# Kernel optimization log

Measured on AMD Instinct MI355X. Metric: run time of the kernel, lower is better.

## Reference

```python
import jax, jax.numpy as jnp
import numpy as np

TOPK = 10  # keep N // TOPK largest scores per query row
EPS = 1e-10


def setup_inputs() -> dict:
    key = jax.random.key(0)
    ks = jax.random.split(key, 8)
    B, C, H, W = 4, 64, 64, 64
    KD, OD = 32, 64  # key_dim, out_dim (out_dim must equal C for residual/view)
    x = jax.random.normal(ks[0], (B, C, H, W), jnp.float32)
    s = 0.05
    Wq = jax.random.normal(ks[1], (KD, C), jnp.float32) * s
    bq = jax.random.normal(ks[2], (KD,), jnp.float32) * s
    Wk = jax.random.normal(ks[3], (KD, C), jnp.float32) * s
    bk = jax.random.normal(ks[4], (KD,), jnp.float32) * s
    Wv = jax.random.normal(ks[5], (OD, C), jnp.float32) * s
    bv = jax.random.normal(ks[6], (OD,), jnp.float32) * s
    gamma = jnp.full((1,), 0.5, jnp.float32)  # torch init is 0; nonzero so output != x
    return {"x": x, "Wq": Wq, "bq": bq, "Wk": Wk, "bk": bk, "Wv": Wv, "bv": bv, "gamma": gamma}


def reference(x, Wq, bq, Wk, bk, Wv, bv, gamma):
    B, C, H, W = x.shape
    N = H * W
    xf = x.reshape(B, C, N)
    # 1x1 convs == per-pixel linear projections
    q = jnp.einsum('kc,bcn->bnk', Wq, xf) + bq                 # [B, N, KD]
    k = jnp.einsum('kc,bcn->bkn', Wk, xf) + bk[:, None]        # [B, KD, N]
    v = jnp.einsum('vc,bcn->bvn', Wv, xf) + bv[:, None]        # [B, OD, N]
    energy = jnp.einsum('bnk,bkm->bnm', q, k)                  # [B, N, N]
    kk = N // TOPK
    _, idx = jax.lax.top_k(energy, kk)                         # [B, N, kk]
    # scatter 1.0 at top-k positions along last dim
    bi = jnp.arange(B)[:, None, None]
    ri = jnp.arange(N)[None, :, None]
    mask = jnp.zeros_like(energy).at[bi, ri, idx].set(1.0)
    # mask_softmax: max over FULL row (matches torch code), exp, mask, renormalize
    m = jnp.max(energy, axis=-1, keepdims=True)
    e = jnp.exp(energy - m) * mask
    attn = e / (jnp.sum(e, axis=-1, keepdims=True) + EPS)      # [B, N, N]
    # bmm(value, attention^T): out[b,v,i] = sum_j v[b,v,j] * attn[b,i,j]
    out = jnp.einsum('bvj,bij->bvi', v, attn)                  # [B, OD, N]
    return (gamma[0] * out + xf).reshape(B, C, H, W)
```

## Files before the change

### kernel.cpp

```cpp
#include <hip/hip_runtime.h>

#define BATCH 4
#define CCH   64
#define NPIX  4096
#define KD    32
#define OD    64
#define KK    409
#define EPSF  1e-10f

__global__ __launch_bounds__(256, 4) void qkv_kernel(
    const float* __restrict__ x,
    const float* __restrict__ Wq, const float* __restrict__ bq,
    const float* __restrict__ Wk, const float* __restrict__ bk,
    const float* __restrict__ Wv, const float* __restrict__ bv,
    float* __restrict__ Q, float* __restrict__ Km, float* __restrict__ Vm)
{
    __shared__ float xt[64][65];
    __shared__ float wat[64][36];
    __shared__ float wbt[64][36];
    __shared__ float ba_s[32], bb_s[32];

    int tid = threadIdx.x;
    int bx  = blockIdx.x;
    bool vmode = bx >= 256;
    int tile = vmode ? bx - 256 : bx;
    int b    = tile >> 6;
    int n0   = (tile & 63) << 6;

    for (int i = tid; i < 64 * 64; i += 256) {
        int c = i >> 6, p = i & 63;
        xt[c][p] = x[((size_t)b * CCH + c) * NPIX + n0 + p];
    }
    if (!vmode) {
        for (int i = tid; i < 2048; i += 256) {
            int o = i >> 6, c = i & 63;
            wat[c][o] = Wq[i];
            wbt[c][o] = Wk[i];
        }
        if (tid < 32) { ba_s[tid] = bq[tid]; bb_s[tid] = bk[tid]; }
    } else {
        for (int i = tid; i < 4096; i += 256) {
            int o = i >> 6, c = i & 63;
            if (o < 32) wat[c][o] = Wv[i]; else wbt[c][o - 32] = Wv[i];
        }
        if (tid < 32) { ba_s[tid] = bv[tid]; bb_s[tid] = bv[tid + 32]; }
    }
    __syncthreads();

    int px  = tid & 63;
    int grp = tid >> 6;
    int n   = n0 + px;
    const float (*wt)[36] = (grp < 2) ? wat : wbt;
    const float* bs = (grp < 2) ? ba_s : bb_s;
    int o0 = (grp & 1) << 4;

    float a[16];
    #pragma unroll
    for (int t = 0; t < 16; ++t) a[t] = bs[o0 + t];

    #pragma unroll 2
    for (int c = 0; c < 64; ++c) {
        float xv = xt[c][px];
        const float4* wr = (const float4*)&wt[c][o0];
        float4 w0 = wr[0], w1 = wr[1], w2 = wr[2], w3 = wr[3];
        a[0]  = fmaf(w0.x, xv, a[0]);  a[1]  = fmaf(w0.y, xv, a[1]);
        a[2]  = fmaf(w0.z, xv, a[2]);  a[3]  = fmaf(w0.w, xv, a[3]);
        a[4]  = fmaf(w1.x, xv, a[4]);  a[5]  = fmaf(w1.y, xv, a[5]);
        a[6]  = fmaf(w1.z, xv, a[6]);  a[7]  = fmaf(w1.w, xv, a[7]);
        a[8]  = fmaf(w2.x, xv, a[8]);  a[9]  = fmaf(w2.y, xv, a[9]);
        a[10] = fmaf(w2.z, xv, a[10]); a[11] = fmaf(w2.w, xv, a[11]);
        a[12] = fmaf(w3.x, xv, a[12]); a[13] = fmaf(w3.y, xv, a[13]);
        a[14] = fmaf(w3.z, xv, a[14]); a[15] = fmaf(w3.w, xv, a[15]);
    }

    if (!vmode) {
        if (grp < 2) {
            #pragma unroll
            for (int t = 0; t < 16; ++t)
                Q[((size_t)b * NPIX + n) * KD + o0 + t] = a[t];
        } else {
            #pragma unroll
            for (int t = 0; t < 16; ++t)
                Km[((size_t)b * KD + o0 + t) * NPIX + n] = a[t];
        }
    } else {
        int ob = ((grp < 2) ? 0 : 32) + o0;
        #pragma unroll
        for (int t = 0; t < 16; ++t)
            Vm[((size_t)b * NPIX + n) * OD + ob + t] = a[t];
    }
}

__global__ __launch_bounds__(512, 4) void attn_kernel(
    const float* __restrict__ x,  const float* __restrict__ Q,
    const float* __restrict__ Km, const float* __restrict__ Vm,
    const float* __restrict__ gamma, float* __restrict__ out)
{
    __shared__ __align__(16) unsigned short ek[8][NPIX];
    __shared__ __align__(16) float qld[KD][8];
    __shared__ __align__(16) unsigned h8[8][256];
    __shared__ unsigned redk0[8][8];
    volatile __shared__ unsigned sh_b8[8], sh_r8[8];

    int tid  = threadIdx.x;
    int lane = tid & 63, wv = tid >> 6;
    int bx   = blockIdx.x;
    int b    = bx >> 9;
    int i0   = (bx & 511) << 3;

    float gscale = gamma[0];

    if (tid < 256) {
        int kd = tid & 31, rr = tid >> 5;
        qld[kd][rr] = Q[((size_t)b * NPIX + i0 + rr) * KD + kd];
    }
    __syncthreads();

    #define EKEY(EV, KV) { KV = (int)fmaf((EV), 4096.0f, 32768.0f); \
                           KV = KV < 0 ? 0 : (KV > 65535 ? 65535 : KV); }

    const float4* Kb4 = (const float4*)(Km + (size_t)b * KD * NPIX);
    unsigned lm0 = 0u, lm1 = 0u, lm2 = 0u, lm3 = 0u,
             lm4 = 0u, lm5 = 0u, lm6 = 0u, lm7 = 0u;
    #pragma unroll 1
    for (int g = 0; g < 2; ++g) {
        int c4 = tid + (g << 9);
        float4 a0 = {0,0,0,0}, a1 = {0,0,0,0}, a2 = {0,0,0,0}, a3 = {0,0,0,0};
        float4 a4 = {0,0,0,0}, a5 = {0,0,0,0}, a6 = {0,0,0,0}, a7 = {0,0,0,0};
        #pragma unroll 4
        for (int kd = 0; kd < KD; ++kd) {
            float4 kv = Kb4[(kd << 10) + c4];
            float4 qA = *(const float4*)&qld[kd][0];
            float4 qB = *(const float4*)&qld[kd][4];
            #define FMA4(A, S) { A.x = fmaf((S), kv.x, A.x); A.y = fmaf((S), kv.y, A.y); \
                                 A.z = fmaf((S), kv.z, A.z); A.w = fmaf((S), kv.w, A.w); }
            FMA4(a0, qA.x) FMA4(a1, qA.y) FMA4(a2, qA.z) FMA4(a3, qA.w)
            FMA4(a4, qB.x) FMA4(a5, qB.y) FMA4(a6, qB.z) FMA4(a7, qB.w)
            #undef FMA4
        }
        #define DOROW(A, R, LM) { int k0,k1,k2,k3; \
            EKEY(A.x,k0); EKEY(A.y,k1); EKEY(A.z,k2); EKEY(A.w,k3); \
            LM = max(LM, (unsigned)max(max(k0,k1),max(k2,k3))); \
            ((ushort4*)ek[R])[c4] = make_ushort4((unsigned short)k0,(unsigned short)k1, \
                                                 (unsigned short)k2,(unsigned short)k3); }
        DOROW(a0,0,lm0) DOROW(a1,1,lm1) DOROW(a2,2,lm2) DOROW(a3,3,lm3)
        DOROW(a4,4,lm4) DOROW(a5,5,lm5) DOROW(a6,6,lm6) DOROW(a7,7,lm7)
        #undef DOROW
    }
    #define RMAX(V, R) { unsigned v_ = (V); \
        _Pragma("unroll") \
        for (int off = 32; off; off >>= 1) \
            v_ = max(v_, (unsigned)__shfl_down((int)v_, off, 64)); \
        if (lane == 0) redk0[wv][R] = v_; }
    RMAX(lm0,0) RMAX(lm1,1) RMAX(lm2,2) RMAX(lm3,3)
    RMAX(lm4,4) RMAX(lm5,5) RMAX(lm6,6) RMAX(lm7,7)
    #undef RMAX
    __syncthreads();

    const int r = wv;
    const int i = i0 + r;
    unsigned mk = 0u;
    #pragma unroll
    for (int w = 0; w < 8; ++w) mk = max(mk, redk0[w][r]);
    const ushort4* ek4 = (const ushort4*)ek[r];
    unsigned* hw = h8[r];

    #define WSCAN(RNEED, OUTB, OUTR) { \
        uint4 hh = *((const uint4*)&hw[lane << 2]); \
        unsigned s3 = hh.w, s2 = hh.w + hh.z, s1 = s2 + hh.y, s0 = s1 + hh.x; \
        unsigned X = s0; \
        _Pragma("unroll") \
        for (int off = 1; off < 64; off <<= 1) { \
            unsigned v = (unsigned)__shfl_down((int)X, off, 64); \
            if (lane + off < 64) X += v; } \
        unsigned Xn = (unsigned)__shfl_down((int)X, 1, 64); \
        if (lane == 63) Xn = 0u; \
        unsigned S0 = X, S1 = Xn + s1, S2 = Xn + s2, S3 = Xn + s3, S4 = Xn; \
        if (S0 >= (RNEED) && S1 < (RNEED)) { sh_b8[r] = (lane << 2) | 0; sh_r8[r] = (RNEED) - S1; } \
        if (S1 >= (RNEED) && S2 < (RNEED)) { sh_b8[r] = (lane << 2) | 1; sh_r8[r] = (RNEED) - S2; } \
        if (S2 >= (RNEED) && S3 < (RNEED)) { sh_b8[r] = (lane << 2) | 2; sh_r8[r] = (RNEED) - S3; } \
        if (S3 >= (RNEED) && S4 < (RNEED)) { sh_b8[r] = (lane << 2) | 3; sh_r8[r] = (RNEED) - S4; } \
        OUTB = sh_b8[r]; OUTR = sh_r8[r]; }

    #pragma unroll
    for (int z = 0; z < 4; ++z) hw[(z << 6) + lane] = 0u;
    #pragma unroll 4
    for (int g = 0; g < 16; ++g) {
        ushort4 kv = ek4[lane + (g << 6)];
        atomicAdd(&hw[kv.x >> 8], 1u);
        atomicAdd(&hw[kv.y >> 8], 1u);
        atomicAdd(&hw[kv.z >> 8], 1u);
        atomicAdd(&hw[kv.w >> 8], 1u);
    }
    unsigned bh, rn;
    WSCAN(KK, bh, rn)

    #pragma unroll
    for (int z = 0; z < 4; ++z) hw[(z << 6) + lane] = 0u;
    #pragma unroll 4
    for (int g = 0; g < 16; ++g) {
        ushort4 kv = ek4[lane + (g << 6)];
        if ((unsigned)(kv.x >> 8) == bh) atomicAdd(&hw[kv.x & 255u], 1u);
        if ((unsigned)(kv.y >> 8) == bh) atomicAdd(&hw[kv.y & 255u], 1u);
        if ((unsigned)(kv.z >> 8) == bh) atomicAdd(&hw[kv.z & 255u], 1u);
        if ((unsigned)(kv.w >> 8) == bh) atomicAdd(&hw[kv.w & 255u], 1u);
    }
    unsigned bl, rt;
    WSCAN(rn, bl, rt)
    #undef WSCAN
    int tu = (int)((bh << 8) | bl);

    unsigned short* selr = (unsigned short*)hw;
    unsigned base = 0u, tbase = 0u;
    float lsum = 0.f;
    #pragma unroll 4
    for (int g = 0; g < 16; ++g) {
        ushort4 kv = ek4[lane + (g << 6)];
        #pragma unroll
        for (int c = 0; c < 4; ++c) {
            int k = (c == 0) ? kv.x : (c == 1) ? kv.y : (c == 2) ? kv.z : kv.w;
            bool tie = (k == tu);
            unsigned long long tmask = __ballot(tie);
            bool sel = (k > tu);
            if (tie) {
                unsigned tix = tbase + (unsigned)__popcll(tmask & ((1ull << lane) - 1ull));
                sel = (tix < rt);
            }
            tbase += (unsigned)__popcll(tmask);
            unsigned long long smask = __ballot(sel);
            if (sel) {
                unsigned pos = base + (unsigned)__popcll(smask & ((1ull << lane) - 1ull));
                int j = ((lane + (g << 6)) << 2) | c;
                selr[pos] = (unsigned short)j;
                lsum += __expf((float)(k - (int)mk) * 0.000244140625f);
            }
            base += (unsigned)__popcll(smask);
        }
    }
    #pragma unroll
    for (int off = 32; off; off >>= 1) lsum += __shfl_xor(lsum, off, 64);
    float denom = lsum + EPSF;

    int eslot = lane >> 4, vq = lane & 15;
    const float4* Vb4 = (const float4*)(Vm + (size_t)b * NPIX * OD);
    const unsigned short* ekr = ek[r];
    float4 acc = make_float4(0.f, 0.f, 0.f, 0.f);
    #pragma unroll 2
    for (int s0 = 0; s0 < KK; s0 += 4) {
        int s = s0 + eslot;
        if (s < KK) {
            int j = selr[s];
            int k = ekr[j];
            float w = __expf((float)(k - (int)mk) * 0.000244140625f);
            float4 v4 = Vb4[(j << 4) + vq];
            acc.x = fmaf(w, v4.x, acc.x);
            acc.y = fmaf(w, v4.y, acc.y);
            acc.z = fmaf(w, v4.z, acc.z);
            acc.w = fmaf(w, v4.w, acc.w);
        }
    }
    #pragma unroll
    for (int off = 16; off <= 32; off <<= 1) {
        acc.x += __shfl_xor(acc.x, off, 64);
        acc.y += __shfl_xor(acc.y, off, 64);
        acc.z += __shfl_xor(acc.z, off, 64);
        acc.w += __shfl_xor(acc.w, off, 64);
    }
    if (lane < 16) {
        float sc = gscale / denom;
        size_t basei = ((size_t)b * CCH + (vq << 2)) * NPIX + i;
        out[basei]            = fmaf(sc, acc.x, x[basei]);
        out[basei +   NPIX]   = fmaf(sc, acc.y, x[basei +   NPIX]);
        out[basei + 2*NPIX]   = fmaf(sc, acc.z, x[basei + 2*NPIX]);
        out[basei + 3*NPIX]   = fmaf(sc, acc.w, x[basei + 3*NPIX]);
    }
}

extern "C" void kernel_launch(void* const* d_in, const int* in_sizes, int n_in,
                              void* d_out, int out_size, void* d_ws, size_t ws_size,
                              hipStream_t stream) {
    const float* x     = (const float*)d_in[0];
    const float* Wq    = (const float*)d_in[1];
    const float* bq    = (const float*)d_in[2];
    const float* Wk    = (const float*)d_in[3];
    const float* bk    = (const float*)d_in[4];
    const float* Wv    = (const float*)d_in[5];
    const float* bv    = (const float*)d_in[6];
    const float* gamma = (const float*)d_in[7];
    float* out = (float*)d_out;

    float* Q  = (float*)d_ws;
    float* Km = Q  + (size_t)BATCH * NPIX * KD;
    float* Vm = Km + (size_t)BATCH * KD * NPIX;

    qkv_kernel<<<512, 256, 0, stream>>>(x, Wq, bq, Wk, bk, Wv, bv, Q, Km, Vm);
    attn_kernel<<<BATCH * (NPIX / 8), 512, 0, stream>>>(x, Q, Km, Vm, gamma, out);
}
```

Before: 317.5 us.

## Fuse coarse histogram into QK score pass and pack index with bf16 weight

The coarse 256-bin histogram is now built with shared-memory atomics while the quantized scores are written in the first pass, removing a separate per-row rescan of the key buffer. The histogram array grows to 412 slots so it can later hold the packed selection list, where each entry stores the column index together with a bf16-rounded exp weight. The PV loop then reads one word per selected element instead of an index lookup, a key reread and a recomputed exp. In exchange, atomics move into the compute phase, where all 512 threads contend on the same bins, and the weights lose precision to bf16 while the denominator still sums full-precision values.

```diff
diff --git a/kernel.cpp b/kernel.cpp
--- a/kernel.cpp
+++ b/kernel.cpp
@@ -7,6 +7,7 @@
 #define OD    64
 #define KK    409
 #define EPSF  1e-10f
+#define HSLOT 412
 
 __global__ __launch_bounds__(256, 4) void qkv_kernel(
     const float* __restrict__ x,
@@ -98,7 +99,7 @@
 {
     __shared__ __align__(16) unsigned short ek[8][NPIX];
     __shared__ __align__(16) float qld[KD][8];
-    __shared__ __align__(16) unsigned h8[8][256];
+    __shared__ __align__(16) unsigned h8[8][HSLOT];
     __shared__ unsigned redk0[8][8];
     volatile __shared__ unsigned sh_b8[8], sh_r8[8];
 
@@ -110,6 +111,7 @@
 
     float gscale = gamma[0];
 
+    for (int z = tid; z < 8 * HSLOT; z += 512) (&h8[0][0])[z] = 0u;
     if (tid < 256) {
         int kd = tid & 31, rr = tid >> 5;
         qld[kd][rr] = Q[((size_t)b * NPIX + i0 + rr) * KD + kd];
@@ -142,7 +144,11 @@
             EKEY(A.x,k0); EKEY(A.y,k1); EKEY(A.z,k2); EKEY(A.w,k3); \
             LM = max(LM, (unsigned)max(max(k0,k1),max(k2,k3))); \
             ((ushort4*)ek[R])[c4] = make_ushort4((unsigned short)k0,(unsigned short)k1, \
-                                                 (unsigned short)k2,(unsigned short)k3); }
+                                                 (unsigned short)k2,(unsigned short)k3); \
+            atomicAdd(&h8[R][k0 >> 8], 1u); \
+            atomicAdd(&h8[R][k1 >> 8], 1u); \
+            atomicAdd(&h8[R][k2 >> 8], 1u); \
+            atomicAdd(&h8[R][k3 >> 8], 1u); }
         DOROW(a0,0,lm0) DOROW(a1,1,lm1) DOROW(a2,2,lm2) DOROW(a3,3,lm3)
         DOROW(a4,4,lm4) DOROW(a5,5,lm5) DOROW(a6,6,lm6) DOROW(a7,7,lm7)
         #undef DOROW
@@ -182,16 +188,6 @@
         if (S3 >= (RNEED) && S4 < (RNEED)) { sh_b8[r] = (lane << 2) | 3; sh_r8[r] = (RNEED) - S4; } \
         OUTB = sh_b8[r]; OUTR = sh_r8[r]; }
 
-    #pragma unroll
-    for (int z = 0; z < 4; ++z) hw[(z << 6) + lane] = 0u;
-    #pragma unroll 4
-    for (int g = 0; g < 16; ++g) {
-        ushort4 kv = ek4[lane + (g << 6)];
-        atomicAdd(&hw[kv.x >> 8], 1u);
-        atomicAdd(&hw[kv.y >> 8], 1u);
-        atomicAdd(&hw[kv.z >> 8], 1u);
-        atomicAdd(&hw[kv.w >> 8], 1u);
-    }
     unsigned bh, rn;
     WSCAN(KK, bh, rn)
 
@@ -210,7 +206,7 @@
     #undef WSCAN
     int tu = (int)((bh << 8) | bl);
 
-    unsigned short* selr = (unsigned short*)hw;
+    unsigned* selw32 = hw;
     unsigned base = 0u, tbase = 0u;
     float lsum = 0.f;
     #pragma unroll 4
@@ -231,8 +227,10 @@
             if (sel) {
                 unsigned pos = base + (unsigned)__popcll(smask & ((1ull << lane) - 1ull));
                 int j = ((lane + (g << 6)) << 2) | c;
-                selr[pos] = (unsigned short)j;
-                lsum += __expf((float)(k - (int)mk) * 0.000244140625f);
+                float w = __expf((float)(k - (int)mk) * 0.000244140625f);
+                lsum += w;
+                selw32[pos] = ((unsigned)j << 16) |
+                              ((__float_as_uint(w) + 0x8000u) >> 16);
             }
             base += (unsigned)__popcll(smask);
         }
@@ -243,15 +241,14 @@
 
     int eslot = lane >> 4, vq = lane & 15;
     const float4* Vb4 = (const float4*)(Vm + (size_t)b * NPIX * OD);
-    const unsigned short* ekr = ek[r];
     float4 acc = make_float4(0.f, 0.f, 0.f, 0.f);
     #pragma unroll 2
     for (int s0 = 0; s0 < KK; s0 += 4) {
         int s = s0 + eslot;
         if (s < KK) {
-            int j = selr[s];
-            int k = ekr[j];
-            float w = __expf((float)(k - (int)mk) * 0.000244140625f);
+            unsigned pk = selw32[s];
+            float w = __uint_as_float(pk << 16);
+            int j   = (int)(pk >> 16);
             float4 v4 = Vb4[(j << 4) + vq];
             acc.x = fmaf(w, v4.x, acc.x);
             acc.y = fmaf(w, v4.y, acc.y);
```

New measurement: 311.2 us. -2.0%, faster.
